# Kernel tuning notes

Measured on AMD Instinct MI355X. Metric: run time of the kernel, lower is better.

Reference implementation:

```python
import jax, jax.numpy as jnp
import numpy as np

GATE_DECAY = 3.0

def setup_inputs() -> dict:
    key = jax.random.key(0)
    ks = jax.random.split(key, 4)
    B, S, D, I = 8, 2048, 512, 2048
    x = jax.random.normal(ks[0], (B, S, D), dtype=jnp.float32)
    # kaiming normal fan_in, linear gain: std = 1/sqrt(fan_in)
    Wa = jax.random.normal(ks[1], (I, D), dtype=jnp.float32) / np.sqrt(D)
    Wi = jax.random.normal(ks[2], (I, D), dtype=jnp.float32) / np.sqrt(D)
    ba = jnp.zeros((I,), dtype=jnp.float32)
    bi = jnp.zeros((I,), dtype=jnp.float32)
    lo, hi = np.log(0.9 / 0.1), np.log(0.999 / 0.001)  # logit(0.9), logit(0.999)
    gate = jax.random.uniform(ks[3], (I,), dtype=jnp.float32, minval=lo, maxval=hi)
    return {"x": x, "Wa": Wa, "ba": ba, "Wi": Wi, "bi": bi, "gate": gate}

def reference(x, Wa, ba, Wi, bi, gate):
    # Precompute both projections for all timesteps as large GEMMs.
    pa = jnp.einsum('bsd,id->bsi', x, Wa) + ba   # [B,S,I]
    pi = jnp.einsum('bsd,id->bsi', x, Wi) + bi   # [B,S,I]
    reset_gate = jax.nn.sigmoid(pa)
    input_gate = jax.nn.sigmoid(pi)
    alpha = jax.nn.sigmoid(gate)                  # [I]
    adaptive_alpha = alpha / (GATE_DECAY ** reset_gate)          # [B,S,I]
    drive = jnp.sqrt(1.0 - adaptive_alpha ** 2) * (input_gate * pi)
    B, S, I = pa.shape

    def step(h, ac):
        a, c = ac
        h = a * h + c
        return h, h

    h0 = jnp.zeros((B, I), dtype=x.dtype)
    # scan over time: move S to leading axis
    _, ys = jax.lax.scan(step, h0, (adaptive_alpha.transpose(1, 0, 2), drive.transpose(1, 0, 2)))
    return ys.transpose(1, 0, 2)  # [B,S,I]
```

## Files before the change

### kernel.cpp

```cpp
#include <hip/hip_runtime.h>


#define LOG2_3 1.5849625007211562f

typedef _Float16 f16x8 __attribute__((ext_vector_type(8)));
typedef _Float16 f16x4 __attribute__((ext_vector_type(4)));
typedef _Float16 f16x2 __attribute__((ext_vector_type(2)));
typedef float f32x4 __attribute__((ext_vector_type(4)));

__device__ __forceinline__ float sigmoidf_(float v) {
  return 1.0f / (1.0f + __expf(-v));
}

__device__ __forceinline__ void async_copy16(void* lds, const void* gp) {
  __builtin_amdgcn_global_load_lds((__attribute__((address_space(1))) void*)gp,
                                   (__attribute__((address_space(3))) void*)lds,
                                   16, 0, 0);
}

__global__ __launch_bounds__(256) void cvt_all(const float* __restrict__ x,
                                               const float* __restrict__ Wa,
                                               const float* __restrict__ Wi,
                                               _Float16* __restrict__ xh,
                                               _Float16* __restrict__ wh) {
  int idx = blockIdx.x * 256 + threadIdx.x;
  const float* src;
  _Float16* dst;
  int off;
  if (idx < 2097152) {
    src = x; dst = xh; off = idx;
  } else if (idx < 2097152 + 262144) {
    src = Wa; dst = wh; off = idx - 2097152;
  } else {
    src = Wi; dst = wh + 1048576; off = idx - 2359296;
  }
  float4 v = ((const float4*)src)[off];
  f16x4 h;
  h[0] = (_Float16)v.x;
  h[1] = (_Float16)v.y;
  h[2] = (_Float16)v.z;
  h[3] = (_Float16)v.w;
  ((f16x4*)dst)[off] = h;
}

__global__ __launch_bounds__(256) void gemm_xw(const _Float16* __restrict__ Ah,
                                               const _Float16* __restrict__ Wh,
                                               const float* __restrict__ ba,
                                               const float* __restrict__ bi,
                                               _Float16* __restrict__ P) {
  constexpr int K = 512;
  constexpr int N2 = 4096;
  __shared__ __align__(16) _Float16 smem[8704];
  _Float16* As = smem;
  _Float16* Bs = smem + 4096;
  const int t = threadIdx.x;
  const int mBase = blockIdx.y * 128;
  const int nBase = blockIdx.x * 128;
  const int r = t >> 2;
  const int c8 = (t & 3) * 8;
  const _Float16* gA0 = Ah + (size_t)(mBase + r) * K + c8;
  const _Float16* gB0 = Wh + (size_t)(nBase + r) * K + c8;
  _Float16* lA0 = As + r * 32 + c8;
  _Float16* lB0 = Bs + r * 32 + c8;

  const int lane = t & 63;
  const int wave = t >> 6;
  const int wm = (wave & 1) * 64;
  const int wn = (wave >> 1) * 64;
  const int lrow = lane & 15;
  const int quad = lane >> 4;

  f32x4 acc[4][4];
#pragma unroll
  for (int i = 0; i < 4; ++i)
#pragma unroll
    for (int j = 0; j < 4; ++j)
      acc[i][j] = (f32x4)0.0f;

  for (int kt = 0; kt < K; kt += 32) {
    async_copy16(lA0, gA0 + kt);
    async_copy16(lA0 + 64 * 32, gA0 + (size_t)64 * K + kt);
    async_copy16(lB0, gB0 + kt);
    async_copy16(lB0 + 64 * 32, gB0 + (size_t)64 * K + kt);
    __syncthreads();
    f16x8 af[4], bf[4];
#pragma unroll
    for (int i = 0; i < 4; ++i)
      af[i] = *(const f16x8*)(As + (wm + i * 16 + lrow) * 32 + quad * 8);
#pragma unroll
    for (int j = 0; j < 4; ++j)
      bf[j] = *(const f16x8*)(Bs + (wn + j * 16 + lrow) * 32 + quad * 8);
#pragma unroll
    for (int i = 0; i < 4; ++i)
#pragma unroll
      for (int j = 0; j < 4; ++j)
        acc[i][j] = __builtin_amdgcn_mfma_f32_16x16x32_f16(af[i], bf[j], acc[i][j], 0, 0, 0);
    __syncthreads();
  }

  float bias[4];
#pragma unroll
  for (int j = 0; j < 4; ++j) {
    const int n = nBase + wn + j * 16 + lrow;
    bias[j] = (n < 2048) ? ba[n] : bi[n - 2048];
  }

  const int row_r = t >> 4;
  const int col8 = (t & 15) * 8;
#pragma unroll
  for (int h = 0; h < 2; ++h) {
    if (wm == h * 64) {
#pragma unroll
      for (int i = 0; i < 4; ++i)
#pragma unroll
        for (int j = 0; j < 4; ++j)
#pragma unroll
          for (int rr = 0; rr < 4; ++rr)
            smem[(i * 16 + quad * 4 + rr) * 136 + wn + j * 16 + lrow] =
                (_Float16)(acc[i][j][rr] + bias[j]);
    }
    __syncthreads();
#pragma unroll
    for (int it = 0; it < 4; ++it) {
      const int m_loc = it * 16 + row_r;
      f16x8 v = *(const f16x8*)(smem + m_loc * 136 + col8);
      *(f16x8*)(P + (size_t)(mBase + h * 64 + m_loc) * N2 + nBase + col8) = v;
    }
    __syncthreads();
  }
}

__device__ __forceinline__ void gate_ac(float pa, float pi, float alpha, float& a, float& c) {
  float rg = sigmoidf_(pa);
  a = alpha * exp2f(-LOG2_3 * rg);
  float ig = sigmoidf_(pi);
  c = sqrtf(fmaxf(1.0f - a * a, 0.0f)) * (ig * pi);
}

__global__ __launch_bounds__(256) void scan_pass1(const _Float16* __restrict__ P,
                                                  const float* __restrict__ gate,
                                                  float2* __restrict__ agg) {
  const int tt = blockIdx.x * 256 + threadIdx.x;
  const int i0 = tt * 2;
  const int ch = blockIdx.y;
  const int b = blockIdx.z;
  const float2 g = ((const float2*)gate)[tt];
  const float al0 = sigmoidf_(g.x);
  const float al1 = sigmoidf_(g.y);
  const _Float16* row = P + ((size_t)(b * 2048 + ch * 32)) * 4096 + i0;
  float A0 = 1.0f, H0 = 0.0f, A1 = 1.0f, H1 = 0.0f;
  for (int s4 = 0; s4 < 8; ++s4) {
    f16x2 pa2[4], pi2[4];
#pragma unroll
    for (int u = 0; u < 4; ++u) {
      pa2[u] = *(const f16x2*)(row + (size_t)u * 4096);
      pi2[u] = *(const f16x2*)(row + (size_t)u * 4096 + 2048);
    }
    row += 4 * 4096;
#pragma unroll
    for (int u = 0; u < 4; ++u) {
      float a, c;
      gate_ac((float)pa2[u][0], (float)pi2[u][0], al0, a, c);
      A0 *= a;
      H0 = fmaf(a, H0, c);
      gate_ac((float)pa2[u][1], (float)pi2[u][1], al1, a, c);
      A1 *= a;
      H1 = fmaf(a, H1, c);
    }
  }
  float4 o;
  o.x = A0; o.y = H0; o.z = A1; o.w = H1;
  ((float4*)agg)[((size_t)(b * 64 + ch)) * 1024 + tt] = o;
}

__global__ __launch_bounds__(64) void scan_pass2(const float2* __restrict__ agg,
                                                 float* __restrict__ carry) {
  const int i = blockIdx.x * 64 + threadIdx.x;
  const int b = blockIdx.y;
  float h = 0.0f;
  for (int c8 = 0; c8 < 8; ++c8) {
    float2 aH[8];
#pragma unroll
    for (int u = 0; u < 8; ++u)
      aH[u] = agg[((size_t)(b * 64 + c8 * 8 + u)) * 2048 + i];
#pragma unroll
    for (int u = 0; u < 8; ++u) {
      carry[((size_t)(b * 64 + c8 * 8 + u)) * 2048 + i] = h;
      h = fmaf(aH[u].x, h, aH[u].y);
    }
  }
}

__global__ __launch_bounds__(256) void scan_pass3(const _Float16* __restrict__ P,
                                                  const float* __restrict__ gate,
                                                  const float* __restrict__ carry,
                                                  float* __restrict__ out) {
  const int tt = blockIdx.x * 256 + threadIdx.x;
  const int i0 = tt * 2;
  const int ch = blockIdx.y;
  const int b = blockIdx.z;
  const float2 g = ((const float2*)gate)[tt];
  const float al0 = sigmoidf_(g.x);
  const float al1 = sigmoidf_(g.y);
  const float2 cr = ((const float2*)(carry + ((size_t)(b * 64 + ch)) * 2048))[tt];
  float h0 = cr.x, h1 = cr.y;
  const _Float16* row = P + ((size_t)(b * 2048 + ch * 32)) * 4096 + i0;
  float* orow = out + ((size_t)(b * 2048 + ch * 32)) * 2048 + i0;
  for (int s4 = 0; s4 < 8; ++s4) {
    f16x2 pa2[4], pi2[4];
#pragma unroll
    for (int u = 0; u < 4; ++u) {
      pa2[u] = *(const f16x2*)(row + (size_t)u * 4096);
      pi2[u] = *(const f16x2*)(row + (size_t)u * 4096 + 2048);
    }
    row += 4 * 4096;
#pragma unroll
    for (int u = 0; u < 4; ++u) {
      float a, c;
      gate_ac((float)pa2[u][0], (float)pi2[u][0], al0, a, c);
      h0 = fmaf(a, h0, c);
      gate_ac((float)pa2[u][1], (float)pi2[u][1], al1, a, c);
      h1 = fmaf(a, h1, c);
      float2 o;
      o.x = h0; o.y = h1;
      *(float2*)(orow + (size_t)u * 2048) = o;
    }
    orow += 4 * 2048;
  }
}

extern "C" void kernel_launch(void* const* d_in, const int* in_sizes, int n_in,
                              void* d_out, int out_size, void* d_ws, size_t ws_size,
                              hipStream_t stream) {
  const float* x = (const float*)d_in[0];
  const float* Wa = (const float*)d_in[1];
  const float* ba = (const float*)d_in[2];
  const float* Wi = (const float*)d_in[3];
  const float* bi = (const float*)d_in[4];
  const float* gate = (const float*)d_in[5];
  float* out = (float*)d_out;

  char* ws = (char*)d_ws;
  _Float16* xh = (_Float16*)ws;
  _Float16* wh = (_Float16*)(ws + 16777216);
  const size_t MN2 = (size_t)16384 * 4096;
  _Float16* P = (_Float16*)(ws + 20971520);
  float2* agg = (float2*)(ws + 20971520 + MN2 * 2);
  float* carry = (float*)(ws + 20971520 + MN2 * 2 + 8388608);

  cvt_all<<<10240, 256, 0, stream>>>(x, Wa, Wi, xh, wh);
  gemm_xw<<<dim3(32, 128), 256, 0, stream>>>(xh, wh, ba, bi, P);
  scan_pass1<<<dim3(4, 64, 8), 256, 0, stream>>>(P, gate, agg);
  scan_pass2<<<dim3(32, 8), 64, 0, stream>>>(agg, carry);
  scan_pass3<<<dim3(4, 64, 8), 256, 0, stream>>>(P, gate, carry, out);
}
```

Measured before the change: 378.7 us.

## Fuse gate math and chunk-local scan aggregation into GEMM epilogue

Interleaves the Wa and Wi rows in the converted weight buffer so each GEMM tile holds matching pa/pi column pairs. The GEMM epilogue then computes the decay a and drive c, writes them as fp16 pairs, and reduces per-chunk (A,H) aggregates directly. This removes the separate scan_pass1 kernel and its full re-read of the projection buffer. The final pass only does FMAs on the precomputed a,c. The cost is a heavier epilogue with serial per-thread loops, and a and c are now stored in fp16, which may lose precision.

```diff
diff --git a/kernel.cpp b/kernel.cpp
--- a/kernel.cpp
+++ b/kernel.cpp
@@ -26,13 +26,15 @@
   int idx = blockIdx.x * 256 + threadIdx.x;
   const float* src;
   _Float16* dst;
-  int off;
+  int off, doff;
   if (idx < 2097152) {
-    src = x; dst = xh; off = idx;
+    src = x; dst = xh; off = idx; doff = idx;
   } else if (idx < 2097152 + 262144) {
     src = Wa; dst = wh; off = idx - 2097152;
+    doff = off + ((off >> 7) << 7);
   } else {
-    src = Wi; dst = wh + 1048576; off = idx - 2359296;
+    src = Wi; dst = wh; off = idx - 2359296;
+    doff = off + ((off >> 7) << 7) + 128;
   }
   float4 v = ((const float4*)src)[off];
   f16x4 h;
@@ -40,17 +42,28 @@
   h[1] = (_Float16)v.y;
   h[2] = (_Float16)v.z;
   h[3] = (_Float16)v.w;
-  ((f16x4*)dst)[off] = h;
-}
-
-__global__ __launch_bounds__(256) void gemm_xw(const _Float16* __restrict__ Ah,
-                                               const _Float16* __restrict__ Wh,
-                                               const float* __restrict__ ba,
-                                               const float* __restrict__ bi,
-                                               _Float16* __restrict__ P) {
+  ((f16x4*)dst)[doff] = h;
+}
+
+__device__ __forceinline__ void gate_ac(float pa, float pi, float alpha, float& a, float& c) {
+  float rg = sigmoidf_(pa);
+  a = alpha * exp2f(-LOG2_3 * rg);
+  float ig = sigmoidf_(pi);
+  c = sqrtf(fmaxf(1.0f - a * a, 0.0f)) * (ig * pi);
+}
+
+__global__ __launch_bounds__(256) void gemm_gate(const _Float16* __restrict__ Ah,
+                                                 const _Float16* __restrict__ Wh,
+                                                 const float* __restrict__ ba,
+                                                 const float* __restrict__ bi,
+                                                 const float* __restrict__ gate,
+                                                 _Float16* __restrict__ AC,
+                                                 float2* __restrict__ agg) {
   constexpr int K = 512;
   constexpr int N2 = 4096;
   __shared__ __align__(16) _Float16 smem[8704];
+  __shared__ float pAs[8 * 65];
+  __shared__ float pHs[8 * 65];
   _Float16* As = smem;
   _Float16* Bs = smem + 4096;
   const int t = threadIdx.x;
@@ -102,11 +115,14 @@
 #pragma unroll
   for (int j = 0; j < 4; ++j) {
     const int n = nBase + wn + j * 16 + lrow;
-    bias[j] = (n < 2048) ? ba[n] : bi[n - 2048];
-  }
-
-  const int row_r = t >> 4;
-  const int col8 = (t & 15) * 8;
+    bias[j] = (n & 1) ? bi[n >> 1] : ba[n >> 1];
+  }
+
+  const int col = t & 63;
+  const int q = t >> 6;
+  const float alpha = sigmoidf_(gate[(nBase >> 1) + col]);
+  const int b = blockIdx.y >> 4;
+
 #pragma unroll
   for (int h = 0; h < 2; ++h) {
     if (wm == h * 64) {
@@ -120,57 +136,36 @@
                 (_Float16)(acc[i][j][rr] + bias[j]);
     }
     __syncthreads();
-#pragma unroll
-    for (int it = 0; it < 4; ++it) {
-      const int m_loc = it * 16 + row_r;
-      f16x8 v = *(const f16x8*)(smem + m_loc * 136 + col8);
-      *(f16x8*)(P + (size_t)(mBase + h * 64 + m_loc) * N2 + nBase + col8) = v;
-    }
-    __syncthreads();
-  }
-}
-
-__device__ __forceinline__ void gate_ac(float pa, float pi, float alpha, float& a, float& c) {
-  float rg = sigmoidf_(pa);
-  a = alpha * exp2f(-LOG2_3 * rg);
-  float ig = sigmoidf_(pi);
-  c = sqrtf(fmaxf(1.0f - a * a, 0.0f)) * (ig * pi);
-}
-
-__global__ __launch_bounds__(256) void scan_pass1(const _Float16* __restrict__ P,
-                                                  const float* __restrict__ gate,
-                                                  float2* __restrict__ agg) {
-  const int tt = blockIdx.x * 256 + threadIdx.x;
-  const int i0 = tt * 2;
-  const int ch = blockIdx.y;
-  const int b = blockIdx.z;
-  const float2 g = ((const float2*)gate)[tt];
-  const float al0 = sigmoidf_(g.x);
-  const float al1 = sigmoidf_(g.y);
-  const _Float16* row = P + ((size_t)(b * 2048 + ch * 32)) * 4096 + i0;
-  float A0 = 1.0f, H0 = 0.0f, A1 = 1.0f, H1 = 0.0f;
-  for (int s4 = 0; s4 < 8; ++s4) {
-    f16x2 pa2[4], pi2[4];
-#pragma unroll
-    for (int u = 0; u < 4; ++u) {
-      pa2[u] = *(const f16x2*)(row + (size_t)u * 4096);
-      pi2[u] = *(const f16x2*)(row + (size_t)u * 4096 + 2048);
-    }
-    row += 4 * 4096;
-#pragma unroll
-    for (int u = 0; u < 4; ++u) {
+    float A = 1.0f, Hn = 0.0f;
+    _Float16* ACp = AC + (size_t)(mBase + h * 64 + q * 16) * N2 + nBase + 2 * col;
+#pragma unroll 4
+    for (int rs = 0; rs < 16; ++rs) {
+      f16x2 pp = *(const f16x2*)(smem + (q * 16 + rs) * 136 + 2 * col);
       float a, c;
-      gate_ac((float)pa2[u][0], (float)pi2[u][0], al0, a, c);
-      A0 *= a;
-      H0 = fmaf(a, H0, c);
-      gate_ac((float)pa2[u][1], (float)pi2[u][1], al1, a, c);
-      A1 *= a;
-      H1 = fmaf(a, H1, c);
-    }
-  }
-  float4 o;
-  o.x = A0; o.y = H0; o.z = A1; o.w = H1;
-  ((float4*)agg)[((size_t)(b * 64 + ch)) * 1024 + tt] = o;
+      gate_ac((float)pp[0], (float)pp[1], alpha, a, c);
+      f16x2 o;
+      o[0] = (_Float16)a;
+      o[1] = (_Float16)c;
+      *(f16x2*)ACp = o;
+      ACp += N2;
+      A *= a;
+      Hn = fmaf(a, Hn, c);
+    }
+    pAs[(h * 4 + q) * 65 + col] = A;
+    pHs[(h * 4 + q) * 65 + col] = Hn;
+    __syncthreads();
+  }
+
+  if (t < 64) {
+#pragma unroll
+    for (int k = 0; k < 4; ++k) {
+      float A0 = pAs[(2 * k) * 65 + t], H0 = pHs[(2 * k) * 65 + t];
+      float A1 = pAs[(2 * k + 1) * 65 + t], H1 = pHs[(2 * k + 1) * 65 + t];
+      const int ch = ((blockIdx.y & 15) << 2) + k;
+      agg[((size_t)(b * 64 + ch)) * 2048 + (nBase >> 1) + t] =
+          make_float2(A0 * A1, fmaf(A1, H0, H1));
+    }
+  }
 }
 
 __global__ __launch_bounds__(64) void scan_pass2(const float2* __restrict__ agg,
@@ -191,38 +186,30 @@
   }
 }
 
-__global__ __launch_bounds__(256) void scan_pass3(const _Float16* __restrict__ P,
-                                                  const float* __restrict__ gate,
-                                                  const float* __restrict__ carry,
-                                                  float* __restrict__ out) {
+__global__ __launch_bounds__(256) void scan_out(const _Float16* __restrict__ AC,
+                                                const float* __restrict__ carry,
+                                                float* __restrict__ out) {
   const int tt = blockIdx.x * 256 + threadIdx.x;
   const int i0 = tt * 2;
   const int ch = blockIdx.y;
   const int b = blockIdx.z;
-  const float2 g = ((const float2*)gate)[tt];
-  const float al0 = sigmoidf_(g.x);
-  const float al1 = sigmoidf_(g.y);
   const float2 cr = ((const float2*)(carry + ((size_t)(b * 64 + ch)) * 2048))[tt];
   float h0 = cr.x, h1 = cr.y;
-  const _Float16* row = P + ((size_t)(b * 2048 + ch * 32)) * 4096 + i0;
+  const _Float16* row = AC + ((size_t)(b * 2048 + ch * 32)) * 4096 + i0 * 2;
   float* orow = out + ((size_t)(b * 2048 + ch * 32)) * 2048 + i0;
   for (int s4 = 0; s4 < 8; ++s4) {
-    f16x2 pa2[4], pi2[4];
+    f16x4 v[4];
+#pragma unroll
+    for (int u = 0; u < 4; ++u)
+      v[u] = *(const f16x4*)(row + (size_t)u * 4096);
+    row += 4 * 4096;
 #pragma unroll
     for (int u = 0; u < 4; ++u) {
-      pa2[u] = *(const f16x2*)(row + (size_t)u * 4096);
-      pi2[u] = *(const f16x2*)(row + (size_t)u * 4096 + 2048);
-    }
-    row += 4 * 4096;
-#pragma unroll
-    for (int u = 0; u < 4; ++u) {
-      float a, c;
-      gate_ac((float)pa2[u][0], (float)pi2[u][0], al0, a, c);
-      h0 = fmaf(a, h0, c);
-      gate_ac((float)pa2[u][1], (float)pi2[u][1], al1, a, c);
-      h1 = fmaf(a, h1, c);
+      h0 = fmaf((float)v[u][0], h0, (float)v[u][1]);
+      h1 = fmaf((float)v[u][2], h1, (float)v[u][3]);
       float2 o;
-      o.x = h0; o.y = h1;
+      o.x = h0;
+      o.y = h1;
       *(float2*)(orow + (size_t)u * 2048) = o;
     }
     orow += 4 * 2048;
@@ -244,13 +231,12 @@
   _Float16* xh = (_Float16*)ws;
   _Float16* wh = (_Float16*)(ws + 16777216);
   const size_t MN2 = (size_t)16384 * 4096;
-  _Float16* P = (_Float16*)(ws + 20971520);
+  _Float16* AC = (_Float16*)(ws + 20971520);
   float2* agg = (float2*)(ws + 20971520 + MN2 * 2);
   float* carry = (float*)(ws + 20971520 + MN2 * 2 + 8388608);
 
   cvt_all<<<10240, 256, 0, stream>>>(x, Wa, Wi, xh, wh);
-  gemm_xw<<<dim3(32, 128), 256, 0, stream>>>(xh, wh, ba, bi, P);
-  scan_pass1<<<dim3(4, 64, 8), 256, 0, stream>>>(P, gate, agg);
+  gemm_gate<<<dim3(32, 128), 256, 0, stream>>>(xh, wh, ba, bi, gate, AC, agg);
   scan_pass2<<<dim3(32, 8), 64, 0, stream>>>(agg, carry);
-  scan_pass3<<<dim3(4, 64, 8), 256, 0, stream>>>(P, gate, carry, out);
-}
+  scan_out<<<dim3(4, 64, 8), 256, 0, stream>>>(AC, carry, out);
+}
```

Result: faster. 356.9 us (-5.8%).
